# Performance work log

Measured on AMD Instinct MI355X. Metric: run time of the kernel, lower is better.

Reference implementation:

```python
import jax, jax.numpy as jnp
import numpy as np

TOP_K = 2  # cfg.num_experts_per_tok
INIT_STD = 0.02


def setup_inputs() -> dict:
    key = jax.random.key(0)
    ks = jax.random.split(key, 6)
    B, S, D, F, E = 4, 2048, 1024, 4096, 8
    return {
        "residual": jax.random.normal(ks[0], (B, S, D), dtype=jnp.float32),
        "W_router": jax.random.normal(ks[1], (E, D), dtype=jnp.float32) * INIT_STD,
        "W_in": jax.random.normal(ks[2], (E, D, F), dtype=jnp.float32) * INIT_STD,
        "b_in": jnp.zeros((E, F), dtype=jnp.float32),
        "W_out": jax.random.normal(ks[3], (E, F, D), dtype=jnp.float32) * INIT_STD,
        "b_out": jnp.zeros((E, D), dtype=jnp.float32),
    }


def reference(residual, W_router, W_in, b_in, W_out, b_out):
    B, S, D = residual.shape
    E = W_router.shape[0]
    x = residual.reshape(-1, D)                      # [T, D], T = B*S

    # Router: softmax over experts, pick top-k, renormalize selected weights.
    logits = jnp.einsum('td,ed->te', x, W_router)    # [T, E]
    probs = jax.nn.softmax(logits, axis=-1)
    top_w, top_i = jax.lax.top_k(probs, TOP_K)       # [T, K]
    top_w = top_w / jnp.sum(top_w, axis=-1, keepdims=True)

    # Dense combine weights [T, E]; zero for non-selected experts.
    combine = jnp.sum(jax.nn.one_hot(top_i, E, dtype=x.dtype) * top_w[..., None], axis=1)

    # Weighted sum of expert MLP outputs (GELU experts, exact erf as in torch).
    y = jnp.zeros_like(x)
    for e in range(E):  # small fixed expert count
        h = jax.nn.gelu(x @ W_in[e] + b_in[e], approximate=False)   # [T, F]
        y = y + combine[:, e:e + 1] * (h @ W_out[e] + b_out[e])     # [T, D]
    return y.reshape(B, S, D)
```

## Files before the change

kernel.cpp:

```cpp
#include <hip/hip_runtime.h>
#include <hip/hip_bf16.h>
#include <math.h>

#define T_TOK 8192
#define DMODEL 1024
#define FFN 4096
#define NEXP 8
#define NSLOT (T_TOK * 2)
#define MAXT 136

typedef _Float16 f16;
typedef _Float16 half8 __attribute__((ext_vector_type(8)));
typedef _Float16 half4 __attribute__((ext_vector_type(4)));
typedef float f32x4 __attribute__((ext_vector_type(4)));
typedef unsigned int u32;

__device__ __forceinline__ void gll16(const void* g, void* l) {
  __builtin_amdgcn_global_load_lds(
      (const __attribute__((address_space(1))) u32*)g,
      (__attribute__((address_space(3))) u32*)l, 16, 0, 0);
}

__device__ __forceinline__ f32x4 ntload4(const float* p) {
  return __builtin_nontemporal_load((const f32x4*)p);
}

__device__ __forceinline__ float gelu_fast(float v) {
  float x = fabsf(v) * 0.70710678118654752f;
  float t = 1.0f / (1.0f + 0.3275911f * x);
  float poly = ((((1.061405429f * t - 1.453152027f) * t + 1.421413741f) * t -
                 0.284496736f) * t + 0.254829592f) * t;
  float erf_ = 1.0f - poly * __expf(-x * x);
  erf_ = copysignf(erf_, v);
  return 0.5f * v * (1.0f + erf_);
}

__device__ __forceinline__ float gelu_exact(float v) {
  return 0.5f * v * (1.0f + erff(v * 0.70710678118654752f));
}

__device__ __forceinline__ void transq_tile(const float* __restrict__ ip,
                                            f16* __restrict__ op, int R, int C,
                                            int r0, int c0, char* smemraw) {
  float* tile = (float*)smemraw;
  int tid = threadIdx.x;
  int q = tid & 15;
  int rr = tid >> 4;
#pragma unroll
  for (int p = 0; p < 8; p++) {
    int row = rr + p * 16;
    f32x4 v = ntload4(ip + (size_t)(r0 + row) * C + c0 + q * 4);
    int qs = (q + (row >> 3)) & 15;
    *(f32x4*)(tile + row * 64 + qs * 4) = v;
  }
  __syncthreads();
#pragma unroll
  for (int p = 0; p < 4; p++) {
    int idx = tid + p * 256;
    int c = idx >> 4;
    int b = idx & 15;
    half8 h;
#pragma unroll
    for (int i = 0; i < 8; i++) {
      int row = b * 8 + i;
      int qs = (((c >> 2) + b) & 15);
      h[i] = (f16)tile[row * 64 + qs * 4 + (c & 3)];
    }
    *(half8*)(op + (size_t)(c0 + c) * R + r0 + b * 8) = h;
  }
}

__global__ __launch_bounds__(256) void prepA_k(
    const float* __restrict__ x, const float* __restrict__ Wr,
    const float* __restrict__ Wi,
    int* __restrict__ sel_e, float* __restrict__ sel_w,
    f16* __restrict__ xh, f16* __restrict__ WiT) {
  __shared__ __align__(16) char smem[32768];
  if (blockIdx.x < 4096) {
    int e = blockIdx.x >> 9;
    int idx = blockIdx.x & 511;
    int rt = idx >> 6, ct = idx & 63;
    transq_tile(Wi + (size_t)e * DMODEL * FFN, WiT + (size_t)e * DMODEL * FFN,
                DMODEL, FFN, rt * 128, ct * 64, smem);
  } else {
    int rb = blockIdx.x - 4096;
    int t = rb * 4 + (threadIdx.x >> 6);
    int lane = threadIdx.x & 63;
    const float* xp = x + (size_t)t * DMODEL;
    f16* xhp = xh + (size_t)t * DMODEL;
    float p[NEXP];
#pragma unroll
    for (int e = 0; e < NEXP; e++) p[e] = 0.f;
#pragma unroll
    for (int q = 0; q < 4; q++) {
      f32x4 xv = ntload4(xp + q * 256 + lane * 4);
      half4 h;
      h[0] = (f16)xv[0]; h[1] = (f16)xv[1]; h[2] = (f16)xv[2]; h[3] = (f16)xv[3];
      *(half4*)(xhp + q * 256 + lane * 4) = h;
#pragma unroll
      for (int e = 0; e < NEXP; e++) {
        const f32x4 wv = *(const f32x4*)(Wr + e * DMODEL + q * 256 + lane * 4);
        p[e] += xv[0] * wv[0] + xv[1] * wv[1] + xv[2] * wv[2] + xv[3] * wv[3];
      }
    }
#pragma unroll
    for (int off = 32; off; off >>= 1) {
#pragma unroll
      for (int e = 0; e < NEXP; e++) p[e] += __shfl_xor(p[e], off);
    }
    if (lane == 0) {
      float l0 = -1e30f, l1 = -1e30f;
      int e0 = 0, e1 = 1;
#pragma unroll
      for (int e = 0; e < NEXP; e++) {
        if (p[e] > l0) { l1 = l0; e1 = e0; l0 = p[e]; e0 = e; }
        else if (p[e] > l1) { l1 = p[e]; e1 = e; }
      }
      float r = expf(l1 - l0);
      float inv = 1.f / (1.f + r);
      sel_e[t * 2] = e0;     sel_w[t * 2] = inv;
      sel_e[t * 2 + 1] = e1; sel_w[t * 2 + 1] = r * inv;
    }
  }
}

__global__ __launch_bounds__(256) void count_sched_k(
    const int* __restrict__ sel_e, int* __restrict__ meta) {
  __shared__ int cnts[NEXP];
  int tid = threadIdx.x;
  if (tid < NEXP) cnts[tid] = 0;
  __syncthreads();
  int c0 = 0, c1 = 0, c2 = 0, c3 = 0, c4 = 0, c5 = 0, c6 = 0, c7 = 0;
  for (int i = tid; i < NSLOT; i += 256) {
    int v = sel_e[i];
    c0 += (v == 0); c1 += (v == 1); c2 += (v == 2); c3 += (v == 3);
    c4 += (v == 4); c5 += (v == 5); c6 += (v == 6); c7 += (v == 7);
  }
#pragma unroll
  for (int off = 32; off; off >>= 1) {
    c0 += __shfl_down(c0, off); c1 += __shfl_down(c1, off);
    c2 += __shfl_down(c2, off); c3 += __shfl_down(c3, off);
    c4 += __shfl_down(c4, off); c5 += __shfl_down(c5, off);
    c6 += __shfl_down(c6, off); c7 += __shfl_down(c7, off);
  }
  if ((tid & 63) == 0) {
    atomicAdd(&cnts[0], c0); atomicAdd(&cnts[1], c1);
    atomicAdd(&cnts[2], c2); atomicAdd(&cnts[3], c3);
    atomicAdd(&cnts[4], c4); atomicAdd(&cnts[5], c5);
    atomicAdd(&cnts[6], c6); atomicAdd(&cnts[7], c7);
  }
  __syncthreads();
  if (tid == 0) {
    int* counts = meta;
    int* fill = meta + 64;
    int* offs = meta + 128;
    int* tE = meta + 256;
    int* tR0 = meta + 512;
    int* tRows = meta + 768;
    int off = 0, nt = 0;
    for (int e = 0; e < NEXP; e++) {
      counts[e] = cnts[e];
      offs[e] = off;
      fill[e] = 0;
      int c = cnts[e];
      for (int t0 = 0; t0 < c; t0 += 128) {
        tE[nt] = e; tR0[nt] = off + t0; tRows[nt] = min(128, c - t0); nt++;
      }
      off += c;
    }
    offs[NEXP] = off;
    for (; nt < MAXT; nt++) tE[nt] = -1;
  }
}

__global__ __launch_bounds__(256) void scatter_k(
    const int* __restrict__ sel_e, const float* __restrict__ sel_w,
    const int* __restrict__ offs, int* fill,
    int* __restrict__ row_tok, float* __restrict__ row_w,
    int* __restrict__ inv) {
  int s = blockIdx.x * 256 + threadIdx.x;
  int e = sel_e[s];
  int pos = atomicAdd(&fill[e], 1);
  int r = offs[e] + pos;
  row_tok[r] = s >> 1;
  row_w[r] = sel_w[s];
  inv[s] = r;
}

__global__ __launch_bounds__(256, 3) void gemm1_k(
    const f16* __restrict__ Xh, const f16* __restrict__ Wt,
    const float* __restrict__ b_in, f16* __restrict__ H,
    const int* __restrict__ meta,
    const float* __restrict__ Wo, f16* __restrict__ WoT) {
  __shared__ __align__(16) char smem[36864];

  if (blockIdx.x >= MAXT * 32) {
    int bid = blockIdx.x - MAXT * 32;
    int e = bid >> 9;
    int idx = bid & 511;
    int rt = idx >> 4, ct = idx & 15;
    transq_tile(Wo + (size_t)e * DMODEL * FFN, WoT + (size_t)e * DMODEL * FFN,
                FFN, DMODEL, rt * 128, ct * 64, smem);
    return;
  }
  int bid2 = blockIdx.x;
  int xcd = bid2 & 7, bidx = bid2 >> 3;
  int wg = xcd * ((MAXT * 32) >> 3) + bidx;
  int tm = wg >> 5;
  int n0 = (wg & 31) * 128;
  int e = (meta + 256)[tm];
  if (e < 0) return;
  int row0 = (meta + 512)[tm];
  int nrows = (meta + 768)[tm];
  const int* row_tok = meta + 1024 + 2 * NSLOT;

  int tid = threadIdx.x, lane = tid & 63, wid = tid >> 6;
  int wrow = wid >> 1, wcol = wid & 1;
  int l15 = lane & 15, l4 = lane >> 4;

  u32 aoffs[4], boffs[4];
#pragma unroll
  for (int p = 0; p < 4; p++) {
    int L = tid + p * 256;
    int row = L >> 3, ch = L & 7;
    int cs = ch ^ (row & 7);
    aoffs[p] = (u32)(row_tok[min(row0 + row, NSLOT - 1)] * (DMODEL * 2) + cs * 16);
    boffs[p] = (u32)((e * FFN + n0 + row) * (DMODEL * 2) + cs * 16);
  }
  const char* gA = (const char*)Xh;
  const char* gB = (const char*)Wt;

  f32x4 acc[4][4];
#pragma unroll
  for (int m = 0; m < 4; m++)
#pragma unroll
    for (int n = 0; n < 4; n++) acc[m][n] = (f32x4)0.f;

  const int NT = DMODEL / 64;
  for (int kt = 0; kt < NT; ++kt) {
#pragma unroll
    for (int p = 0; p < 4; p++) {
      gll16(gA + aoffs[p], smem + (tid + p * 256) * 16);
      gll16(gB + boffs[p], smem + 16384 + (tid + p * 256) * 16);
      aoffs[p] += 128; boffs[p] += 128;
    }
    __syncthreads();
#pragma unroll
    for (int s = 0; s < 2; s++) {
      int swz = ((s * 4 + l4) ^ (l15 & 7)) << 4;
      const char* pA = smem + (wrow * 64 + l15) * 128 + swz;
      const char* pB = smem + 16384 + (wcol * 64 + l15) * 128 + swz;
      half8 a[4], b[4];
#pragma unroll
      for (int i = 0; i < 4; i++) a[i] = *(const half8*)(pA + i * 2048);
#pragma unroll
      for (int j = 0; j < 4; j++) b[j] = *(const half8*)(pB + j * 2048);
#pragma unroll
      for (int i = 0; i < 4; i++)
#pragma unroll
        for (int j = 0; j < 4; j++)
          acc[i][j] = __builtin_amdgcn_mfma_f32_16x16x32_f16(a[i], b[j], acc[i][j], 0, 0, 0);
    }
    __syncthreads();
  }

  char* wsm = smem + wid * 9216;
  float bias[4];
#pragma unroll
  for (int n = 0; n < 4; n++) bias[n] = b_in[e * FFN + n0 + wcol * 64 + n * 16 + l15];
#pragma unroll
  for (int m = 0; m < 4; m++)
#pragma unroll
    for (int n = 0; n < 4; n++)
#pragma unroll
      for (int j = 0; j < 4; j++) {
        int lrow = m * 16 + l4 * 4 + j;
        *(f16*)(wsm + lrow * 144 + (n * 16 + l15) * 2) =
            (f16)gelu_fast(acc[m][n][j] + bias[n]);
      }
#pragma unroll
  for (int p = 0; p < 8; ++p) {
    int lr = (lane >> 3) + p * 8;
    if (wrow * 64 + lr < nrows) {
      f32x4 v = *(const f32x4*)(wsm + lr * 144 + (lane & 7) * 16);
      __builtin_nontemporal_store(
          v, (f32x4*)(H + (size_t)(row0 + wrow * 64 + lr) * FFN + n0 +
                      wcol * 64 + (lane & 7) * 8));
    }
  }
}

__global__ __launch_bounds__(256, 3) void gemm2_k(
    const f16* __restrict__ H, const f16* __restrict__ Wt,
    const float* __restrict__ b_out, f16* __restrict__ Y0,
    f16* __restrict__ Y1, const int* __restrict__ meta) {
  int xcd = blockIdx.x & 7, bidx = blockIdx.x >> 3;
  int wg = xcd * (gridDim.x >> 3) + bidx;
  int tm = wg >> 4;
  int r4 = wg & 15;
  int n0 = (r4 & 7) * 128;
  int ks = r4 >> 3;
  int e = (meta + 256)[tm];
  if (e < 0) return;
  int row0 = (meta + 512)[tm];
  int nrows = (meta + 768)[tm];

  __shared__ __align__(16) char smem[36864];

  int tid = threadIdx.x, lane = tid & 63, wid = tid >> 6;
  int wrow = wid >> 1, wcol = wid & 1;
  int l15 = lane & 15, l4 = lane >> 4;
  u32 k0b = (u32)(ks * (FFN / 2) * 2);

  u32 aoffs[4], boffs[4];
#pragma unroll
  for (int p = 0; p < 4; p++) {
    int L = tid + p * 256;
    int row = L >> 3, ch = L & 7;
    int cs = ch ^ (row & 7);
    aoffs[p] = (u32)((u32)min(row0 + row, NSLOT - 1) * (FFN * 2) + k0b + cs * 16);
    boffs[p] = (u32)((u32)(e * DMODEL + n0 + row) * (FFN * 2) + k0b + cs * 16);
  }
  const char* gA = (const char*)H;
  const char* gB = (const char*)Wt;

  f32x4 acc[4][4];
#pragma unroll
  for (int m = 0; m < 4; m++)
#pragma unroll
    for (int n = 0; n < 4; n++) acc[m][n] = (f32x4)0.f;

  const int NT = (FFN / 2) / 64;
  for (int kt = 0; kt < NT; ++kt) {
#pragma unroll
    for (int p = 0; p < 4; p++) {
      gll16(gA + aoffs[p], smem + (tid + p * 256) * 16);
      gll16(gB + boffs[p], smem + 16384 + (tid + p * 256) * 16);
      aoffs[p] += 128; boffs[p] += 128;
    }
    __syncthreads();
#pragma unroll
    for (int s = 0; s < 2; s++) {
      int swz = ((s * 4 + l4) ^ (l15 & 7)) << 4;
      const char* pA = smem + (wrow * 64 + l15) * 128 + swz;
      const char* pB = smem + 16384 + (wcol * 64 + l15) * 128 + swz;
      half8 a[4], b[4];
#pragma unroll
      for (int i = 0; i < 4; i++) a[i] = *(const half8*)(pA + i * 2048);
#pragma unroll
      for (int j = 0; j < 4; j++) b[j] = *(const half8*)(pB + j * 2048);
#pragma unroll
      for (int i = 0; i < 4; i++)
#pragma unroll
        for (int j = 0; j < 4; j++)
          acc[i][j] = __builtin_amdgcn_mfma_f32_16x16x32_f16(a[i], b[j], acc[i][j], 0, 0, 0);
    }
    __syncthreads();
  }

  f16* Y = ks ? Y1 : Y0;
  char* wsm = smem + wid * 9216;
  float bias[4];
#pragma unroll
  for (int n = 0; n < 4; n++)
    bias[n] = (ks == 0) ? b_out[e * DMODEL + n0 + wcol * 64 + n * 16 + l15] : 0.f;
#pragma unroll
  for (int m = 0; m < 4; m++)
#pragma unroll
    for (int n = 0; n < 4; n++)
#pragma unroll
      for (int j = 0; j < 4; j++) {
        int lrow = m * 16 + l4 * 4 + j;
        *(f16*)(wsm + lrow * 144 + (n * 16 + l15) * 2) =
            (f16)(acc[m][n][j] + bias[n]);
      }
#pragma unroll
  for (int p = 0; p < 8; ++p) {
    int lr = (lane >> 3) + p * 8;
    if (wrow * 64 + lr < nrows) {
      f32x4 v = *(const f32x4*)(wsm + lr * 144 + (lane & 7) * 16);
      __builtin_nontemporal_store(
          v, (f32x4*)(Y + (size_t)(row0 + wrow * 64 + lr) * DMODEL + n0 +
                      wcol * 64 + (lane & 7) * 8));
    }
  }
}

__global__ __launch_bounds__(256) void combine_k(
    const f16* __restrict__ Y0, const f16* __restrict__ Y1,
    const int* __restrict__ inv, const float* __restrict__ row_w,
    float* __restrict__ out) {
  int t = blockIdx.x * 4 + (threadIdx.x >> 6);
  int lane = threadIdx.x & 63;
  int r0 = inv[2 * t], r1 = inv[2 * t + 1];
  float w0 = row_w[r0], w1 = row_w[r1];
  int d0 = lane * 16;
  const half8* a0 = (const half8*)(Y0 + (size_t)r0 * DMODEL + d0);
  const half8* a1 = (const half8*)(Y1 + (size_t)r0 * DMODEL + d0);
  const half8* b0 = (const half8*)(Y0 + (size_t)r1 * DMODEL + d0);
  const half8* b1 = (const half8*)(Y1 + (size_t)r1 * DMODEL + d0);
  float* op = out + (size_t)t * DMODEL + d0;
#pragma unroll
  for (int q = 0; q < 2; q++) {
    half8 x0 = a0[q], x1 = a1[q], y0 = b0[q], y1 = b1[q];
    float r[8];
#pragma unroll
    for (int i = 0; i < 8; i++)
      r[i] = w0 * ((float)x0[i] + (float)x1[i]) +
             w1 * ((float)y0[i] + (float)y1[i]);
    f32x4 v1 = {r[0], r[1], r[2], r[3]};
    f32x4 v2 = {r[4], r[5], r[6], r[7]};
    *(f32x4*)(op + q * 8) = v1;
    *(f32x4*)(op + q * 8 + 4) = v2;
  }
}

__global__ __launch_bounds__(256) void naive_k(
    const float* __restrict__ x, const float* __restrict__ W_in,
    const float* __restrict__ b_in, const float* __restrict__ W_out,
    const float* __restrict__ b_out, const int* __restrict__ sel_e,
    const float* __restrict__ sel_w, float* __restrict__ out) {
  int s = blockIdx.x;
  int t = s >> 1;
  int e = sel_e[s];
  float w = sel_w[s];
  __shared__ float xs[DMODEL];
  __shared__ float hs[FFN];
  int tid = threadIdx.x;
  for (int d = tid; d < DMODEL; d += 256) xs[d] = x[(size_t)t * DMODEL + d];
  __syncthreads();
  for (int f = tid; f < FFN; f += 256) {
    float a = b_in[e * FFN + f];
    const float* wp = W_in + (size_t)e * DMODEL * FFN + f;
    for (int d = 0; d < DMODEL; d++) a += xs[d] * wp[(size_t)d * FFN];
    hs[f] = gelu_exact(a);
  }
  __syncthreads();
  for (int d = tid; d < DMODEL; d += 256) {
    float a = b_out[e * DMODEL + d];
    const float* wp = W_out + (size_t)e * FFN * DMODEL + d;
    for (int f = 0; f < FFN; f++) a += hs[f] * wp[(size_t)f * DMODEL];
    atomicAdd(&out[(size_t)t * DMODEL + d], w * a);
  }
}

__global__ __launch_bounds__(256) void router_k(
    const float* __restrict__ x, const float* __restrict__ Wr,
    int* __restrict__ sel_e, float* __restrict__ sel_w) {
  int t = blockIdx.x * 4 + (threadIdx.x >> 6);
  int lane = threadIdx.x & 63;
  const float* xp = x + (size_t)t * DMODEL;
  float p[NEXP];
#pragma unroll
  for (int e = 0; e < NEXP; e++) p[e] = 0.f;
#pragma unroll
  for (int i = 0; i < DMODEL / 64; i++) {
    float xv = xp[lane + i * 64];
#pragma unroll
    for (int e = 0; e < NEXP; e++) p[e] += xv * Wr[e * DMODEL + lane + i * 64];
  }
#pragma unroll
  for (int off = 32; off; off >>= 1) {
#pragma unroll
    for (int e = 0; e < NEXP; e++) p[e] += __shfl_xor(p[e], off);
  }
  if (lane == 0) {
    float l0 = -1e30f, l1 = -1e30f;
    int e0 = 0, e1 = 1;
#pragma unroll
    for (int e = 0; e < NEXP; e++) {
      if (p[e] > l0) { l1 = l0; e1 = e0; l0 = p[e]; e0 = e; }
      else if (p[e] > l1) { l1 = p[e]; e1 = e; }
    }
    float r = expf(l1 - l0);
    float inv = 1.f / (1.f + r);
    sel_e[t * 2] = e0;     sel_w[t * 2] = inv;
    sel_e[t * 2 + 1] = e1; sel_w[t * 2 + 1] = r * inv;
  }
}

extern "C" void kernel_launch(void* const* d_in, const int* in_sizes, int n_in,
                              void* d_out, int out_size, void* d_ws, size_t ws_size,
                              hipStream_t stream) {
  const float* residual = (const float*)d_in[0];
  const float* W_router = (const float*)d_in[1];
  const float* W_in = (const float*)d_in[2];
  const float* b_in = (const float*)d_in[3];
  const float* W_out = (const float*)d_in[4];
  const float* b_out = (const float*)d_in[5];
  float* out = (float*)d_out;

  char* ws = (char*)d_ws;
  int* meta = (int*)ws;
  size_t off = (size_t)1 << 20;
  f16* Xh = (f16*)(ws + off); off += (size_t)T_TOK * DMODEL * 2;
  f16* Wih = (f16*)(ws + off); off += (size_t)NEXP * DMODEL * FFN * 2;
  f16* Woh = (f16*)(ws + off); off += (size_t)NEXP * DMODEL * FFN * 2;
  f16* H = (f16*)(ws + off); off += (size_t)NSLOT * FFN * 2;
  off += 65536;
  bool fast = ws_size >= off;

  f16* Y0 = Wih;
  f16* Y1 = Wih + (size_t)NSLOT * DMODEL;

  int* sel_e = meta + 1024;
  float* sel_w = (float*)(meta + 1024 + NSLOT);
  int* row_tok = meta + 1024 + 2 * NSLOT;
  float* row_w = (float*)(meta + 1024 + 3 * NSLOT);
  int* inv = meta + 1024 + 4 * NSLOT;

  if (fast) {
    prepA_k<<<4096 + T_TOK / 4, 256, 0, stream>>>(
        residual, W_router, W_in, sel_e, sel_w, Xh, Wih);
    count_sched_k<<<1, 256, 0, stream>>>(sel_e, meta);
    scatter_k<<<NSLOT / 256, 256, 0, stream>>>(sel_e, sel_w, meta + 128, meta + 64,
                                               row_tok, row_w, inv);
    gemm1_k<<<MAXT * 32 + 4096, 256, 0, stream>>>(Xh, Wih, b_in, H, meta,
                                                  W_out, Woh);
    gemm2_k<<<MAXT * 16, 256, 0, stream>>>(H, Woh, b_out, Y0, Y1, meta);
    combine_k<<<T_TOK / 4, 256, 0, stream>>>(Y0, Y1, inv, row_w, out);
  } else {
    hipMemsetAsync(d_out, 0, (size_t)out_size * sizeof(float), stream);
    router_k<<<T_TOK / 4, 256, 0, stream>>>(residual, W_router, sel_e, sel_w);
    naive_k<<<NSLOT, 256, 0, stream>>>(residual, W_in, b_in, W_out, b_out,
                                       sel_e, sel_w, out);
  }
}
```

Baseline: 519.7 us.

## Parallelize expert counting and derive tile schedule on the fly in GEMMs

Replaces the single-block count/schedule kernel with a 64-block counting kernel that uses shared and global atomics, plus a memset that zeroes the counters. Each GEMM block now derives its expert, row offset and row count from the counts instead of reading a precomputed tile table, and the scatter kernel computes expert offsets inline. It also swaps nontemporal loads for regular loads and makes the transposed weight stores nontemporal. This aims to remove the serial single-block scheduling step, at the cost of an extra memset launch and a small amount of redundant decode work in every block.

```diff
diff --git a/kernel.cpp b/kernel.cpp
--- a/kernel.cpp
+++ b/kernel.cpp
@@ -19,10 +19,6 @@
   __builtin_amdgcn_global_load_lds(
       (const __attribute__((address_space(1))) u32*)g,
       (__attribute__((address_space(3))) u32*)l, 16, 0, 0);
-}
-
-__device__ __forceinline__ f32x4 ntload4(const float* p) {
-  return __builtin_nontemporal_load((const f32x4*)p);
 }
 
 __device__ __forceinline__ float gelu_fast(float v) {
@@ -39,6 +35,24 @@
   return 0.5f * v * (1.0f + erff(v * 0.70710678118654752f));
 }
 
+__device__ __forceinline__ bool decode_tile(const int* __restrict__ counts,
+                                            int tm, int& e, int& row0,
+                                            int& nrows) {
+  int acc = 0, off = 0;
+#pragma unroll
+  for (int i = 0; i < NEXP; i++) {
+    int c = counts[i];
+    int nt = (c + 127) >> 7;
+    if (tm < acc + nt) {
+      int lt = tm - acc;
+      e = i; row0 = off + lt * 128; nrows = min(128, c - lt * 128);
+      return true;
+    }
+    acc += nt; off += c;
+  }
+  return false;
+}
+
 __device__ __forceinline__ void transq_tile(const float* __restrict__ ip,
                                             f16* __restrict__ op, int R, int C,
                                             int r0, int c0, char* smemraw) {
@@ -49,7 +63,7 @@
 #pragma unroll
   for (int p = 0; p < 8; p++) {
     int row = rr + p * 16;
-    f32x4 v = ntload4(ip + (size_t)(r0 + row) * C + c0 + q * 4);
+    f32x4 v = *(const f32x4*)(ip + (size_t)(r0 + row) * C + c0 + q * 4);
     int qs = (q + (row >> 3)) & 15;
     *(f32x4*)(tile + row * 64 + qs * 4) = v;
   }
@@ -66,7 +80,7 @@
       int qs = (((c >> 2) + b) & 15);
       h[i] = (f16)tile[row * 64 + qs * 4 + (c & 3)];
     }
-    *(half8*)(op + (size_t)(c0 + c) * R + r0 + b * 8) = h;
+    __builtin_nontemporal_store(h, (half8*)(op + (size_t)(c0 + c) * R + r0 + b * 8));
   }
 }
 
@@ -93,7 +107,7 @@
     for (int e = 0; e < NEXP; e++) p[e] = 0.f;
 #pragma unroll
     for (int q = 0; q < 4; q++) {
-      f32x4 xv = ntload4(xp + q * 256 + lane * 4);
+      f32x4 xv = *(const f32x4*)(xp + q * 256 + lane * 4);
       half4 h;
       h[0] = (f16)xv[0]; h[1] = (f16)xv[1]; h[2] = (f16)xv[2]; h[3] = (f16)xv[3];
       *(half4*)(xhp + q * 256 + lane * 4) = h;
@@ -124,64 +138,30 @@
   }
 }
 
-__global__ __launch_bounds__(256) void count_sched_k(
-    const int* __restrict__ sel_e, int* __restrict__ meta) {
-  __shared__ int cnts[NEXP];
+__global__ __launch_bounds__(256) void count64_k(const int* __restrict__ sel_e,
+                                                 int* __restrict__ counts) {
+  __shared__ int lc[NEXP];
   int tid = threadIdx.x;
-  if (tid < NEXP) cnts[tid] = 0;
+  if (tid < NEXP) lc[tid] = 0;
   __syncthreads();
-  int c0 = 0, c1 = 0, c2 = 0, c3 = 0, c4 = 0, c5 = 0, c6 = 0, c7 = 0;
-  for (int i = tid; i < NSLOT; i += 256) {
-    int v = sel_e[i];
-    c0 += (v == 0); c1 += (v == 1); c2 += (v == 2); c3 += (v == 3);
-    c4 += (v == 4); c5 += (v == 5); c6 += (v == 6); c7 += (v == 7);
-  }
-#pragma unroll
-  for (int off = 32; off; off >>= 1) {
-    c0 += __shfl_down(c0, off); c1 += __shfl_down(c1, off);
-    c2 += __shfl_down(c2, off); c3 += __shfl_down(c3, off);
-    c4 += __shfl_down(c4, off); c5 += __shfl_down(c5, off);
-    c6 += __shfl_down(c6, off); c7 += __shfl_down(c7, off);
-  }
-  if ((tid & 63) == 0) {
-    atomicAdd(&cnts[0], c0); atomicAdd(&cnts[1], c1);
-    atomicAdd(&cnts[2], c2); atomicAdd(&cnts[3], c3);
-    atomicAdd(&cnts[4], c4); atomicAdd(&cnts[5], c5);
-    atomicAdd(&cnts[6], c6); atomicAdd(&cnts[7], c7);
-  }
+  int v = sel_e[blockIdx.x * 256 + tid];
+  atomicAdd(&lc[v], 1);
   __syncthreads();
-  if (tid == 0) {
-    int* counts = meta;
-    int* fill = meta + 64;
-    int* offs = meta + 128;
-    int* tE = meta + 256;
-    int* tR0 = meta + 512;
-    int* tRows = meta + 768;
-    int off = 0, nt = 0;
-    for (int e = 0; e < NEXP; e++) {
-      counts[e] = cnts[e];
-      offs[e] = off;
-      fill[e] = 0;
-      int c = cnts[e];
-      for (int t0 = 0; t0 < c; t0 += 128) {
-        tE[nt] = e; tR0[nt] = off + t0; tRows[nt] = min(128, c - t0); nt++;
-      }
-      off += c;
-    }
-    offs[NEXP] = off;
-    for (; nt < MAXT; nt++) tE[nt] = -1;
-  }
+  if (tid < NEXP) atomicAdd(&counts[tid], lc[tid]);
 }
 
 __global__ __launch_bounds__(256) void scatter_k(
     const int* __restrict__ sel_e, const float* __restrict__ sel_w,
-    const int* __restrict__ offs, int* fill,
+    const int* __restrict__ counts, int* fill,
     int* __restrict__ row_tok, float* __restrict__ row_w,
     int* __restrict__ inv) {
   int s = blockIdx.x * 256 + threadIdx.x;
   int e = sel_e[s];
+  int offs = 0;
+#pragma unroll
+  for (int i = 0; i < NEXP; i++) offs += (i < e) ? counts[i] : 0;
   int pos = atomicAdd(&fill[e], 1);
-  int r = offs[e] + pos;
+  int r = offs + pos;
   row_tok[r] = s >> 1;
   row_w[r] = sel_w[s];
   inv[s] = r;
@@ -208,10 +188,8 @@
   int wg = xcd * ((MAXT * 32) >> 3) + bidx;
   int tm = wg >> 5;
   int n0 = (wg & 31) * 128;
-  int e = (meta + 256)[tm];
-  if (e < 0) return;
-  int row0 = (meta + 512)[tm];
-  int nrows = (meta + 768)[tm];
+  int e, row0, nrows;
+  if (!decode_tile(meta, tm, e, row0, nrows)) return;
   const int* row_tok = meta + 1024 + 2 * NSLOT;
 
   int tid = threadIdx.x, lane = tid & 63, wid = tid >> 6;
@@ -300,10 +278,8 @@
   int r4 = wg & 15;
   int n0 = (r4 & 7) * 128;
   int ks = r4 >> 3;
-  int e = (meta + 256)[tm];
-  if (e < 0) return;
-  int row0 = (meta + 512)[tm];
-  int nrows = (meta + 768)[tm];
+  int e, row0, nrows;
+  if (!decode_tile(meta, tm, e, row0, nrows)) return;
 
   __shared__ __align__(16) char smem[36864];
 
@@ -510,10 +486,11 @@
   int* inv = meta + 1024 + 4 * NSLOT;
 
   if (fast) {
+    hipMemsetAsync(meta, 0, 512, stream);
     prepA_k<<<4096 + T_TOK / 4, 256, 0, stream>>>(
         residual, W_router, W_in, sel_e, sel_w, Xh, Wih);
-    count_sched_k<<<1, 256, 0, stream>>>(sel_e, meta);
-    scatter_k<<<NSLOT / 256, 256, 0, stream>>>(sel_e, sel_w, meta + 128, meta + 64,
+    count64_k<<<NSLOT / 256, 256, 0, stream>>>(sel_e, meta);
+    scatter_k<<<NSLOT / 256, 256, 0, stream>>>(sel_e, sel_w, meta, meta + 64,
                                                row_tok, row_w, inv);
     gemm1_k<<<MAXT * 32 + 4096, 256, 0, stream>>>(Xh, Wih, b_in, H, meta,
                                                   W_out, Woh);
```

Result: no change. 512.6 us (-1.4%).
